# Optimization experiments

Hardware: AMD Instinct MI355X
Metric: run time of the kernel (lower is better)

## Reference

```python
import jax, jax.numpy as jnp
import numpy as np

S, B, E, H, NQ, V, T = 128, 128, 64, 8, 8, 30000, 12
N_RAND_OPS = 30


def _build_random_layer(n_wires, n_ops=N_RAND_OPS, seed=1234):
    # Deterministic stand-in for tq.RandomLayer(n_ops=30): random fixed-angle
    # rotations and CNOTs over the wires.
    rng = np.random.RandomState(seed)
    ops = []
    for _ in range(n_ops):
        kind = rng.randint(4)
        if kind == 3 and n_wires >= 2:
            c = int(rng.randint(n_wires))
            t = int(rng.randint(n_wires - 1))
            if t >= c:
                t += 1
            ops.append(('cnot', c, t, 0.0))
        else:
            g = ('rx', 'ry', 'rz')[kind % 3]
            ops.append((g, int(rng.randint(n_wires)), -1, float(rng.uniform(0.0, 2 * np.pi))))
    return ops

_RAND_OPS = _build_random_layer(H)


def _apply_rot(state, kind, theta, w):
    # state: (N, 2, 2, ..., 2); wire w lives on axis w+1. theta: scalar or (N,).
    th = jnp.asarray(theta, jnp.float32)
    if th.ndim == 1:
        th = th.reshape((-1,) + (1,) * (state.ndim - 2))
    th = th / 2
    a0 = jnp.take(state, 0, axis=w + 1)
    a1 = jnp.take(state, 1, axis=w + 1)
    c, s = jnp.cos(th), jnp.sin(th)
    if kind == 'rx':
        n0, n1 = c * a0 - 1j * s * a1, -1j * s * a0 + c * a1
    elif kind == 'ry':
        n0, n1 = c * a0 - s * a1, s * a0 + c * a1
    else:  # rz
        p = jnp.exp(-1j * th)
        n0, n1 = p * a0, jnp.conj(p) * a1
    return jnp.stack([n0, n1], axis=w + 1)


def _apply_cnot(state, c, t):
    s0 = jnp.take(state, 0, axis=c + 1)
    s1 = jnp.take(state, 1, axis=c + 1)
    t_ax = t + 1 if t < c else t  # target axis after removing control axis
    s1 = jnp.flip(s1, axis=t_ax)
    return jnp.stack([s0, s1], axis=c + 1)


def _measure_z(state):
    probs = jnp.real(state * jnp.conj(state))
    n = state.ndim - 1
    zs = []
    for w in range(n):
        d = jnp.take(probs, 0, axis=w + 1) - jnp.take(probs, 1, axis=w + 1)
        zs.append(d.sum(axis=tuple(range(1, d.ndim))))
    return jnp.stack(zs, axis=1)  # (N, n_wires)


def setup_inputs() -> dict:
    key = jax.random.key(0)
    ks = jax.random.split(key, 10)
    fan_lin = E + H
    return {
        'emb': jax.random.normal(ks[0], (V, E), jnp.float32),
        'Win': jax.random.normal(ks[1], (4, NQ, fan_lin), jnp.float32) / np.sqrt(fan_lin),
        'b_in': jax.random.normal(ks[2], (4, NQ), jnp.float32) * 0.1,
        'phi': jax.random.uniform(ks[3], (4, NQ), jnp.float32, 0.0, 2 * np.pi),
        'Wout': jax.random.normal(ks[4], (4, H, NQ), jnp.float32) / np.sqrt(NQ),
        'b_out': jax.random.normal(ks[5], (4, H), jnp.float32) * 0.1,
        'phiq': jax.random.uniform(ks[6], (H,), jnp.float32, 0.0, 2 * np.pi),
        'Whead': jax.random.normal(ks[7], (T, H), jnp.float32) / np.sqrt(H),
        'b_head': jax.random.normal(ks[8], (T,), jnp.float32) * 0.1,
        'sentence': jax.random.randint(ks[9], (S, B), 0, V, jnp.int64),
    }


def reference(emb, Win, b_in, phi, Wout, b_out, phiq, Whead, b_head, sentence):
    embeds = emb[sentence]  # (S, B, E)
    bsz = sentence.shape[1]
    h0 = jnp.zeros((bsz, H), emb.dtype)
    c0 = jnp.zeros_like(h0)

    def step(carry, x):
        hx, cx = carry
        comb = jnp.concatenate([x, hx], axis=1)  # (B, E+H)
        # QGate closed form: RX(z_i) encode + trainable RX(phi_i) + CNOT chain
        # gives <Z_k> = prod_{j<=k} cos(z_j + phi_j).
        z = jnp.einsum('bf,gqf->bgq', comb, Win) + b_in + phi  # (B,4,NQ)
        q = jnp.cumprod(jnp.cos(z), axis=-1)
        pre = jnp.einsum('bgq,ghq->bgh', q, Wout) + b_out      # (B,4,H)
        f = jax.nn.sigmoid(pre[:, 0])
        i = jax.nn.sigmoid(pre[:, 1])
        g = jnp.tanh(pre[:, 2])
        o = jax.nn.sigmoid(pre[:, 3])
        cx = f * cx + i * g
        hx = o * jnp.tanh(cx)
        return (hx, cx), hx

    _, outs = jax.lax.scan(step, (h0, c0), embeds)  # (S, B, H)
    flat = outs.transpose(1, 0, 2).reshape(-1, H)   # (B*S, H) batch-major (as in source)

    # QFC head: statevector simulation over H wires
    n = H
    N = flat.shape[0]
    state = jnp.zeros((N, 2 ** n), jnp.complex64).at[:, 0].set(1.0)
    state = state.reshape((N,) + (2,) * n)
    for w in range(n):
        state = _apply_rot(state, 'ry', flat[:, w], w)
    for name, a, b, ang in _RAND_OPS:
        if name == 'cnot':
            state = _apply_cnot(state, a, b)
        else:
            state = _apply_rot(state, name, ang, a)
    for w in range(n):
        state = _apply_rot(state, 'rx', phiq[w], w)
    zexp = _measure_z(state)                        # (B*S, H)
    logits = zexp @ Whead.T + b_head
    # faithful to source: view batch-major flat tensor as (seq, batch, T)
    logits = logits.reshape(S, B, T)
    return jax.nn.log_softmax(logits, axis=2)
```

## Files before the change

### kernel.cpp

```cpp
#include <hip/hip_runtime.h>
#include <math.h>
#include <stdint.h>

#define S_    128
#define B_    128
#define E_    64
#define H_    8
#define T_    12
#define FAN_  72
#define NOPS_ 30
#define MAXG_ 30
#define NROWS_ (S_ * B_)

constexpr double CT_PI = 3.14159265358979323846;

constexpr double ct_cos(double x) {
    double t = 1.0, s = 1.0, x2 = x * x;
    for (int k = 1; k <= 20; k++) { t *= -x2 / ((2.0*k - 1.0) * (2.0*k)); s += t; }
    return s;
}
constexpr double ct_sin(double x) {
    double t = x, s = x, x2 = x * x;
    for (int k = 1; k <= 20; k++) { t *= -x2 / ((2.0*k) * (2.0*k + 1.0)); s += t; }
    return s;
}

constexpr void ct_mmul(const double* A, const double* B, double* C) {
    for (int i = 0; i < 2; i++)
        for (int j = 0; j < 2; j++) {
            double rr = 0.0, ii = 0.0;
            for (int k = 0; k < 2; k++) {
                double ar = A[(i*2+k)*2], ai = A[(i*2+k)*2+1];
                double br = B[(k*2+j)*2], bi = B[(k*2+j)*2+1];
                rr += ar*br - ai*bi;
                ii += ar*bi + ai*br;
            }
            C[(i*2+j)*2] = rr; C[(i*2+j)*2+1] = ii;
        }
}

struct CTC {
    int n;
    int type[MAXG_];
    int w1[MAXG_];
    int w2[MAXG_];
    double U[MAXG_][8];
    double initM[8][8];
    double endM[8][8];
};

constexpr CTC build_ct() {
    uint32_t mt[624] = {};
    int idx = 624;
    {
        uint32_t s = 1234u;
        for (int i = 0; i < 624; i++) {
            mt[i] = s;
            s = 1812433253u * (s ^ (s >> 30)) + (uint32_t)i + 1u;
        }
    }
    auto nextf = [&]() -> uint32_t {
        if (idx >= 624) {
            for (int i = 0; i < 624; i++) {
                uint32_t y = (mt[i] & 0x80000000u) | (mt[(i+1)%624] & 0x7fffffffu);
                uint32_t v = mt[(i+397)%624] ^ (y >> 1);
                mt[i] = (y & 1u) ? (v ^ 0x9908b0dfu) : v;
            }
            idx = 0;
        }
        uint32_t y = mt[idx++];
        y ^= y >> 11;
        y ^= (y << 7)  & 0x9d2c5680u;
        y ^= (y << 15) & 0xefc60000u;
        y ^= y >> 18;
        return y;
    };
    auto randint = [&](uint32_t n) -> uint32_t {
        uint32_t rng = n - 1u, mask = rng;
        mask |= mask >> 1; mask |= mask >> 2; mask |= mask >> 4;
        mask |= mask >> 8; mask |= mask >> 16;
        uint32_t v = 0;
        do { v = nextf() & mask; } while (v > rng);
        return v;
    };
    auto uniform2pi = [&]() -> double {
        uint32_t a = nextf() >> 5;
        uint32_t b = nextf() >> 6;
        double d = ((double)a * 67108864.0 + (double)b) / 9007199254740992.0;
        return 2.0 * CT_PI * d;
    };

    int kindA[NOPS_] = {}, aA[NOPS_] = {}, bA[NOPS_] = {};
    double UA[NOPS_][8] = {};
    for (int i = 0; i < NOPS_; i++) {
        uint32_t kind = randint(4);
        if (kind == 3u) {
            int c = (int)randint(8);
            int t = (int)randint(7);
            if (t >= c) t += 1;
            kindA[i] = 1; aA[i] = c; bA[i] = t;
            UA[i][0] = 1.0; UA[i][6] = 1.0;
        } else {
            int g = (int)(kind % 3u);
            int w = (int)randint(8);
            double th = uniform2pi();
            double c = ct_cos(0.5 * th), s = ct_sin(0.5 * th);
            kindA[i] = 0; aA[i] = w; bA[i] = -1;
            if (g == 0)      { UA[i][0]=c;  UA[i][3]=-s; UA[i][5]=-s; UA[i][6]=c; }
            else if (g == 1) { UA[i][0]=c;  UA[i][2]=-s; UA[i][4]= s; UA[i][6]=c; }
            else             { UA[i][0]=c;  UA[i][1]=-s; UA[i][6]= c; UA[i][7]=s; }
        }
    }

    int ikind[MAXG_] = {}, ia[MAXG_] = {}, ib[MAXG_] = {};
    double iU[MAXG_][8] = {};
    int cnt = 0;
    double initM[8][8] = {}, endM[8][8] = {};
    for (int w = 0; w < 8; w++) { initM[w][0] = 1.0; initM[w][6] = 1.0;
                                  endM[w][0]  = 1.0; endM[w][6]  = 1.0; }

    for (int oi = 0; oi < NOPS_; oi++) {
        if (kindA[oi] == 0) {
            int w = aA[oi], k = cnt - 1;
            bool merged = false;
            while (k >= 0) {
                if (ikind[k] == 0) {
                    if (ia[k] == w) {
                        double tmp[8] = {};
                        ct_mmul(UA[oi], iU[k], tmp);
                        for (int j = 0; j < 8; j++) iU[k][j] = tmp[j];
                        merged = true; break;
                    }
                    k--;
                } else {
                    if (w == ia[k] || w == ib[k]) break;
                    k--;
                }
            }
            if (merged) continue;
            if (k < 0) {
                double tmp[8] = {};
                ct_mmul(UA[oi], initM[w], tmp);
                for (int j = 0; j < 8; j++) initM[w][j] = tmp[j];
                continue;
            }
            ikind[cnt] = 0; ia[cnt] = w; ib[cnt] = -1;
            for (int j = 0; j < 8; j++) iU[cnt][j] = UA[oi][j];
            cnt++;
        } else {
            int c = aA[oi], t2 = bA[oi], k = cnt - 1;
            bool cancelled = false;
            while (k >= 0) {
                if (ikind[k] == 0) {
                    int w = ia[k];
                    if (w == c || w == t2) break;
                    k--;
                } else {
                    int c2 = ia[k], tt = ib[k];
                    if (c2 == c && tt == t2) {
                        for (int m = k; m < cnt - 1; m++) {
                            ikind[m] = ikind[m+1]; ia[m] = ia[m+1]; ib[m] = ib[m+1];
                            for (int j = 0; j < 8; j++) iU[m][j] = iU[m+1][j];
                        }
                        cnt--; cancelled = true; break;
                    }
                    if (c2 != t2 && tt != c) k--;
                    else break;
                }
            }
            if (!cancelled) {
                ikind[cnt] = 1; ia[cnt] = c; ib[cnt] = t2;
                for (int j = 0; j < 8; j++) iU[cnt][j] = 0.0;
                iU[cnt][0] = 1.0; iU[cnt][6] = 1.0;
                cnt++;
            }
        }
    }
    bool blocked[8] = {};
    for (int k = cnt - 1; k >= 0; k--) {
        if (ikind[k] == 0) {
            int w = ia[k];
            if (!blocked[w]) {
                double tmp[8] = {};
                ct_mmul(endM[w], iU[k], tmp);
                for (int j = 0; j < 8; j++) endM[w][j] = tmp[j];
                for (int m = k; m < cnt - 1; m++) {
                    ikind[m] = ikind[m+1]; ia[m] = ia[m+1]; ib[m] = ib[m+1];
                    for (int j = 0; j < 8; j++) iU[m][j] = iU[m+1][j];
                }
                cnt--;
            }
        } else {
            blocked[ia[k]] = true; blocked[ib[k]] = true;
        }
    }

    CTC q = {};
    q.n = cnt;
    for (int i = 0; i < cnt; i++) {
        q.type[i] = ikind[i]; q.w1[i] = ia[i]; q.w2[i] = ib[i];
        for (int j = 0; j < 8; j++) q.U[i][j] = iU[i][j];
    }
    for (int w = 0; w < 8; w++)
        for (int j = 0; j < 8; j++) { q.initM[w][j] = initM[w][j]; q.endM[w][j] = endM[w][j]; }
    return q;
}

constexpr CTC CIRC = build_ct();

#define LOG2E_  1.4426950408889634f
#define LOG2E2_ 2.8853900817779268f

__device__ __forceinline__ float fast_sigmoid(float x) {
    return __builtin_amdgcn_rcpf(1.f + __builtin_amdgcn_exp2f(-LOG2E_ * x));
}
__device__ __forceinline__ float fast_tanh(float x) {
    return 1.f - 2.f * __builtin_amdgcn_rcpf(1.f + __builtin_amdgcn_exp2f(LOG2E2_ * x));
}

template<int CTRL>
__device__ __forceinline__ float dppf(float x) {
    union { float f; int i; } u, r;
    u.f = x;
    r.i = __builtin_amdgcn_update_dpp(0, u.i, CTRL, 0xF, 0xF, true);
    return r.f;
}

template<int M>
__device__ __forceinline__ float lane_xor(float x, int lane) {
    if constexpr (M == 1)  return dppf<0xB1>(x);
    else if constexpr (M == 2) return dppf<0x4E>(x);
    else if constexpr (M == 4) {
        float a = dppf<0x104>(x);
        float b = dppf<0x114>(x);
        return (lane & 4) ? b : a;
    }
    else if constexpr (M == 8) return dppf<0x128>(x);
    else return __shfl_xor(x, M, 64);
}

template<int W>
__device__ __forceinline__ float exch(float x, int lane) {
    if constexpr (W == 0) return __shfl_xor(x, 32, 64);
    else if constexpr (W == 1) return __shfl_xor(x, 16, 64);
    else if constexpr (W == 2) return lane_xor<8>(x, lane);
    else if constexpr (W == 3) return lane_xor<4>(x, lane);
    else if constexpr (W == 4) return lane_xor<2>(x, lane);
    else return lane_xor<1>(x, lane);
}

template<int W>
__device__ __forceinline__ int qbit_ct(int lane, int j) {
    if constexpr (W < 6) return (lane >> (5 - W)) & 1;
    else if constexpr (W == 6) return (j >> 1) & 1;
    else return j & 1;
}

__device__ __forceinline__ void pair_rt(float u0, float u1, float u2, float u3,
                                        float u4, float u5, float u6, float u7,
                                        float& a0r, float& a0i, float& a1r, float& a1i) {
    float n0r = u0*a0r - u1*a0i + u2*a1r - u3*a1i;
    float n0i = u0*a0i + u1*a0r + u2*a1i + u3*a1r;
    float n1r = u4*a0r - u5*a0i + u6*a1r - u7*a1i;
    float n1i = u4*a0i + u5*a0r + u6*a1i + u7*a1r;
    a0r = n0r; a0i = n0i; a1r = n1r; a1i = n1i;
}

template<int W>
__device__ __forceinline__ void gate_rt(float u0, float u1, float u2, float u3,
                                        float u4, float u5, float u6, float u7,
                                        int lane, float ar[4], float ai[4]) {
    if constexpr (W < 6) {
        const int b = (lane >> (5 - W)) & 1;
        const float dr  = b ? u6 : u0;
        const float di  = b ? u7 : u1;
        const float onr = b ? u4 : u2;
        const float oni = b ? u5 : u3;
        #pragma unroll
        for (int j = 0; j < 4; j++) {
            float br = exch<W>(ar[j], lane);
            float bi = exch<W>(ai[j], lane);
            float nr = dr * ar[j] - di * ai[j] + onr * br - oni * bi;
            float ni = dr * ai[j] + di * ar[j] + onr * bi + oni * br;
            ar[j] = nr; ai[j] = ni;
        }
    } else if constexpr (W == 6) {
        pair_rt(u0,u1,u2,u3,u4,u5,u6,u7, ar[0], ai[0], ar[2], ai[2]);
        pair_rt(u0,u1,u2,u3,u4,u5,u6,u7, ar[1], ai[1], ar[3], ai[3]);
    } else {
        pair_rt(u0,u1,u2,u3,u4,u5,u6,u7, ar[0], ai[0], ar[1], ai[1]);
        pair_rt(u0,u1,u2,u3,u4,u5,u6,u7, ar[2], ai[2], ar[3], ai[3]);
    }
}

template<int CW, int TW>
__device__ __forceinline__ void cnot_ct(int lane, float ar[4], float ai[4]) {
    if constexpr (TW < 6) {
        #pragma unroll
        for (int j = 0; j < 4; j++) {
            float br = exch<TW>(ar[j], lane);
            float bi = exch<TW>(ai[j], lane);
            int ctrl = qbit_ct<CW>(lane, j);
            ar[j] = ctrl ? br : ar[j];
            ai[j] = ctrl ? bi : ai[j];
        }
    } else if constexpr (TW == 6) {
        int cA = qbit_ct<CW>(lane, 0), cB = qbit_ct<CW>(lane, 1);
        float n0r = cA ? ar[2] : ar[0], n0i = cA ? ai[2] : ai[0];
        float n2r = cA ? ar[0] : ar[2], n2i = cA ? ai[0] : ai[2];
        float n1r = cB ? ar[3] : ar[1], n1i = cB ? ai[3] : ai[1];
        float n3r = cB ? ar[1] : ar[3], n3i = cB ? ai[1] : ai[3];
        ar[0]=n0r; ai[0]=n0i; ar[1]=n1r; ai[1]=n1i;
        ar[2]=n2r; ai[2]=n2i; ar[3]=n3r; ai[3]=n3i;
    } else {
        int cA = qbit_ct<CW>(lane, 0), cB = qbit_ct<CW>(lane, 2);
        float n0r = cA ? ar[1] : ar[0], n0i = cA ? ai[1] : ai[0];
        float n1r = cA ? ar[0] : ar[1], n1i = cA ? ai[0] : ai[1];
        float n2r = cB ? ar[3] : ar[2], n2i = cB ? ai[3] : ai[2];
        float n3r = cB ? ar[2] : ar[3], n3i = cB ? ai[2] : ai[3];
        ar[0]=n0r; ai[0]=n0i; ar[1]=n1r; ai[1]=n1i;
        ar[2]=n2r; ai[2]=n2i; ar[3]=n3r; ai[3]=n3i;
    }
}

template<int I>
__device__ __forceinline__ void gate_op(int lane, float ar[4], float ai[4]) {
    constexpr int w = CIRC.w1[I];
    constexpr float u0 = (float)CIRC.U[I][0], u1 = (float)CIRC.U[I][1];
    constexpr float u2 = (float)CIRC.U[I][2], u3 = (float)CIRC.U[I][3];
    constexpr float u4 = (float)CIRC.U[I][4], u5 = (float)CIRC.U[I][5];
    constexpr float u6 = (float)CIRC.U[I][6], u7 = (float)CIRC.U[I][7];
    gate_rt<w>(u0,u1,u2,u3,u4,u5,u6,u7, lane, ar, ai);
}

template<int I>
__device__ __forceinline__ void run_ops(int lane, float ar[4], float ai[4]) {
    if constexpr (I < CIRC.n) {
        if constexpr (CIRC.type[I] == 0) gate_op<I>(lane, ar, ai);
        else cnot_ct<CIRC.w1[I], CIRC.w2[I]>(lane, ar, ai);
        run_ops<I + 1>(lane, ar, ai);
    }
}

struct V2 { float r0, i0, r1, i1; };
template<int W>
__device__ __forceinline__ V2 init_wire(float th) {
    constexpr float m0 = (float)CIRC.initM[W][0], m1 = (float)CIRC.initM[W][1];
    constexpr float m2 = (float)CIRC.initM[W][2], m3 = (float)CIRC.initM[W][3];
    constexpr float m4 = (float)CIRC.initM[W][4], m5 = (float)CIRC.initM[W][5];
    constexpr float m6 = (float)CIRC.initM[W][6], m7 = (float)CIRC.initM[W][7];
    float c = __cosf(th), s = __sinf(th);
    V2 v;
    v.r0 = m0*c + m2*s; v.i0 = m1*c + m3*s;
    v.r1 = m4*c + m6*s; v.i1 = m5*c + m7*s;
    return v;
}

template<int W>
__device__ __forceinline__ void final_wire(float c, float s, int lane,
                                           float ar[4], float ai[4]) {
    constexpr float E0 = (float)CIRC.endM[W][0], E1 = (float)CIRC.endM[W][1];
    constexpr float E2 = (float)CIRC.endM[W][2], E3 = (float)CIRC.endM[W][3];
    constexpr float E4 = (float)CIRC.endM[W][4], E5 = (float)CIRC.endM[W][5];
    constexpr float E6 = (float)CIRC.endM[W][6], E7 = (float)CIRC.endM[W][7];
    float F0 =  c*E0 + s*E5;
    float F1 =  c*E1 - s*E4;
    float F2 =  c*E2 + s*E7;
    float F3 =  c*E3 - s*E6;
    float F4 =  s*E1 + c*E4;
    float F5 = -s*E0 + c*E5;
    float F6 =  s*E3 + c*E6;
    float F7 = -s*E2 + c*E7;
    gate_rt<W>(F0,F1,F2,F3,F4,F5,F6,F7, lane, ar, ai);
}

__device__ __forceinline__ void bcast8(float v, int lane, float h[8]) {
    float p  = lane_xor<1>(v, lane);
    float a0 = (lane & 1) ? p : v;
    float a1 = (lane & 1) ? v : p;
    float q0 = lane_xor<2>(a0, lane);
    float q1 = lane_xor<2>(a1, lane);
    float b0 = (lane & 2) ? q0 : a0;
    float b1 = (lane & 2) ? q1 : a1;
    float b2 = (lane & 2) ? a0 : q0;
    float b3 = (lane & 2) ? a1 : q1;
    float r0 = lane_xor<4>(b0, lane);
    float r1 = lane_xor<4>(b1, lane);
    float r2 = lane_xor<4>(b2, lane);
    float r3 = lane_xor<4>(b3, lane);
    h[0] = (lane & 4) ? r0 : b0;  h[1] = (lane & 4) ? r1 : b1;
    h[2] = (lane & 4) ? r2 : b2;  h[3] = (lane & 4) ? r3 : b3;
    h[4] = (lane & 4) ? b0 : r0;  h[5] = (lane & 4) ? b1 : r1;
    h[6] = (lane & 4) ? b2 : r2;  h[7] = (lane & 4) ? b3 : r3;
}

__device__ __forceinline__ void bcast8_s2(float v, int lane, float h[8]) {
    float p  = lane_xor<2>(v, lane);
    float a0 = (lane & 2) ? p : v;
    float a1 = (lane & 2) ? v : p;
    float q0 = lane_xor<4>(a0, lane);
    float q1 = lane_xor<4>(a1, lane);
    float b0 = (lane & 4) ? q0 : a0;
    float b1 = (lane & 4) ? q1 : a1;
    float b2 = (lane & 4) ? a0 : q0;
    float b3 = (lane & 4) ? a1 : q1;
    float r0 = lane_xor<8>(b0, lane);
    float r1 = lane_xor<8>(b1, lane);
    float r2 = lane_xor<8>(b2, lane);
    float r3 = lane_xor<8>(b3, lane);
    h[0] = (lane & 8) ? r0 : b0;  h[1] = (lane & 8) ? r1 : b1;
    h[2] = (lane & 8) ? r2 : b2;  h[3] = (lane & 8) ? r3 : b3;
    h[4] = (lane & 8) ? b0 : r0;  h[5] = (lane & 8) ? b1 : r1;
    h[6] = (lane & 8) ? b2 : r2;  h[7] = (lane & 8) ? b3 : r3;
}

__device__ __forceinline__ void qfc_row(const float th[8],
    float cq[8], float sq[8], int lane,
    const float* __restrict__ Whead, const float* __restrict__ b_head,
    float* __restrict__ outrow)
{
    float ar[4], ai[4];
    {
        V2 v0 = init_wire<0>(th[0]);
        V2 v1 = init_wire<1>(th[1]);
        V2 v2 = init_wire<2>(th[2]);
        V2 v3 = init_wire<3>(th[3]);
        V2 v4 = init_wire<4>(th[4]);
        V2 v5 = init_wire<5>(th[5]);
        V2 v6 = init_wire<6>(th[6]);
        V2 v7 = init_wire<7>(th[7]);
        float Pr = 1.f, Pi = 0.f;
        {
            int bit = (lane >> 5) & 1;
            float er = bit ? v0.r1 : v0.r0, ei = bit ? v0.i1 : v0.i0;
            float nr = Pr*er - Pi*ei, ni = Pr*ei + Pi*er; Pr = nr; Pi = ni;
        }
        {
            int bit = (lane >> 4) & 1;
            float er = bit ? v1.r1 : v1.r0, ei = bit ? v1.i1 : v1.i0;
            float nr = Pr*er - Pi*ei, ni = Pr*ei + Pi*er; Pr = nr; Pi = ni;
        }
        {
            int bit = (lane >> 3) & 1;
            float er = bit ? v2.r1 : v2.r0, ei = bit ? v2.i1 : v2.i0;
            float nr = Pr*er - Pi*ei, ni = Pr*ei + Pi*er; Pr = nr; Pi = ni;
        }
        {
            int bit = (lane >> 2) & 1;
            float er = bit ? v3.r1 : v3.r0, ei = bit ? v3.i1 : v3.i0;
            float nr = Pr*er - Pi*ei, ni = Pr*ei + Pi*er; Pr = nr; Pi = ni;
        }
        {
            int bit = (lane >> 1) & 1;
            float er = bit ? v4.r1 : v4.r0, ei = bit ? v4.i1 : v4.i0;
            float nr = Pr*er - Pi*ei, ni = Pr*ei + Pi*er; Pr = nr; Pi = ni;
        }
        {
            int bit = lane & 1;
            float er = bit ? v5.r1 : v5.r0, ei = bit ? v5.i1 : v5.i0;
            float nr = Pr*er - Pi*ei, ni = Pr*ei + Pi*er; Pr = nr; Pi = ni;
        }
        float t0r = Pr*v6.r0 - Pi*v6.i0, t0i = Pr*v6.i0 + Pi*v6.r0;
        float t1r = Pr*v6.r1 - Pi*v6.i1, t1i = Pr*v6.i1 + Pi*v6.r1;
        ar[0] = t0r*v7.r0 - t0i*v7.i0;  ai[0] = t0r*v7.i0 + t0i*v7.r0;
        ar[1] = t0r*v7.r1 - t0i*v7.i1;  ai[1] = t0r*v7.i1 + t0i*v7.r1;
        ar[2] = t1r*v7.r0 - t1i*v7.i0;  ai[2] = t1r*v7.i0 + t1i*v7.r0;
        ar[3] = t1r*v7.r1 - t1i*v7.i1;  ai[3] = t1r*v7.i1 + t1i*v7.r1;
    }

    run_ops<0>(lane, ar, ai);

    final_wire<0>(cq[0], sq[0], lane, ar, ai);
    final_wire<1>(cq[1], sq[1], lane, ar, ai);
    final_wire<2>(cq[2], sq[2], lane, ar, ai);
    final_wire<3>(cq[3], sq[3], lane, ar, ai);
    final_wire<4>(cq[4], sq[4], lane, ar, ai);
    final_wire<5>(cq[5], sq[5], lane, ar, ai);
    final_wire<6>(cq[6], sq[6], lane, ar, ai);
    final_wire<7>(cq[7], sq[7], lane, ar, ai);

    float p0 = ar[0]*ar[0] + ai[0]*ai[0];
    float p1 = ar[1]*ar[1] + ai[1]*ai[1];
    float p2 = ar[2]*ar[2] + ai[2]*ai[2];
    float p3 = ar[3]*ar[3] + ai[3]*ai[3];
    float pt = p0 + p1 + p2 + p3;
    float a6 = p0 + p1 - p2 - p3;
    float a7 = p0 - p1 + p2 - p3;
    {
        float tv;
        tv = lane_xor<1>(pt, lane);  pt = (lane & 1)  ? (tv - pt) : (tv + pt);
        tv = lane_xor<2>(pt, lane);  pt = (lane & 2)  ? (tv - pt) : (tv + pt);
        tv = lane_xor<4>(pt, lane);  pt = (lane & 4)  ? (tv - pt) : (tv + pt);
        tv = lane_xor<8>(pt, lane);  pt = (lane & 8)  ? (tv - pt) : (tv + pt);
        tv = lane_xor<16>(pt, lane); pt = (lane & 16) ? (tv - pt) : (tv + pt);
        tv = lane_xor<32>(pt, lane); pt = (lane & 32) ? (tv - pt) : (tv + pt);
        a6 += lane_xor<1>(a6, lane);  a6 += lane_xor<2>(a6, lane);
        a6 += lane_xor<4>(a6, lane);  a6 += lane_xor<8>(a6, lane);
        a6 += lane_xor<16>(a6, lane); a6 += lane_xor<32>(a6, lane);
        a7 += lane_xor<1>(a7, lane);  a7 += lane_xor<2>(a7, lane);
        a7 += lane_xor<4>(a7, lane);  a7 += lane_xor<8>(a7, lane);
        a7 += lane_xor<16>(a7, lane); a7 += lane_xor<32>(a7, lane);
    }
    float zl[8];
    zl[0] = __shfl(pt, 32, 64);
    zl[1] = __shfl(pt, 16, 64);
    zl[2] = __shfl(pt, 8, 64);
    zl[3] = __shfl(pt, 4, 64);
    zl[4] = __shfl(pt, 2, 64);
    zl[5] = __shfl(pt, 1, 64);
    zl[6] = a6;
    zl[7] = a7;

    float logit = -1e30f;
    if (lane < T_) {
        logit = b_head[lane];
        #pragma unroll
        for (int w = 0; w < 8; w++)
            logit = fmaf(zl[w], Whead[lane * 8 + w], logit);
    }
    float mx = logit;
    mx = fmaxf(mx, lane_xor<1>(mx, lane));
    mx = fmaxf(mx, lane_xor<2>(mx, lane));
    mx = fmaxf(mx, lane_xor<4>(mx, lane));
    mx = fmaxf(mx, lane_xor<8>(mx, lane));
    float e = (lane < T_) ? __expf(logit - mx) : 0.f;
    float se = e;
    se += lane_xor<1>(se, lane);
    se += lane_xor<2>(se, lane);
    se += lane_xor<4>(se, lane);
    se += lane_xor<8>(se, lane);
    if (lane < T_)
        outrow[lane] = logit - mx - __logf(se);
}

__global__ __launch_bounds__(256) void k_lstm(
    const float* __restrict__ emb,
    const int* __restrict__ sentence,
    const float* __restrict__ Win,
    const float* __restrict__ b_in,
    const float* __restrict__ phi,
    const float* __restrict__ Wout,
    const float* __restrict__ b_out,
    float* __restrict__ angles)
{
    __shared__ float zxs[S_][32];

    const int t  = threadIdx.x;
    const int hw = t >> 5;
    const int l  = t & 31;
    const int b  = blockIdx.x;

    {
        const float4* w4 = (const float4*)(Win + l * FAN_);
        const float cb = b_in[l] + phi[l];

        #pragma unroll
        for (int kk = 0; kk < 4; kk++) {
            const int sb = hw * 16 + kk * 4;
            const float4* e4_0 = (const float4*)(emb + sentence[(sb + 0) * B_ + b] * E_);
            const float4* e4_1 = (const float4*)(emb + sentence[(sb + 1) * B_ + b] * E_);
            const float4* e4_2 = (const float4*)(emb + sentence[(sb + 2) * B_ + b] * E_);
            const float4* e4_3 = (const float4*)(emb + sentence[(sb + 3) * B_ + b] * E_);
            float a0 = cb, a1 = cb, a2 = cb, a3 = cb;
            #pragma unroll
            for (int f = 0; f < 16; f++) {
                float4 wv = w4[f];
                float4 x0 = e4_0[f];
                float4 x1 = e4_1[f];
                float4 x2 = e4_2[f];
                float4 x3 = e4_3[f];
                a0 = fmaf(x0.x, wv.x, a0); a0 = fmaf(x0.y, wv.y, a0);
                a0 = fmaf(x0.z, wv.z, a0); a0 = fmaf(x0.w, wv.w, a0);
                a1 = fmaf(x1.x, wv.x, a1); a1 = fmaf(x1.y, wv.y, a1);
                a1 = fmaf(x1.z, wv.z, a1); a1 = fmaf(x1.w, wv.w, a1);
                a2 = fmaf(x2.x, wv.x, a2); a2 = fmaf(x2.y, wv.y, a2);
                a2 = fmaf(x2.z, wv.z, a2); a2 = fmaf(x2.w, wv.w, a2);
                a3 = fmaf(x3.x, wv.x, a3); a3 = fmaf(x3.y, wv.y, a3);
                a3 = fmaf(x3.z, wv.z, a3); a3 = fmaf(x3.w, wv.w, a3);
            }
            zxs[sb + 0][l] = a0;
            zxs[sb + 1][l] = a1;
            zxs[sb + 2][l] = a2;
            zxs[sb + 3][l] = a3;
        }
    }
    __syncthreads();

    if (t < 16) {
        const int j = t & 1;
        const int q = t >> 1;
        const int rowA = j * 8 + q;
        const int rowB = (j + 2) * 8 + q;

        float whA[8], whB[8], woA[8], woB[8];
        #pragma unroll
        for (int k = 0; k < 8; k++) {
            whA[k] = Win[rowA * FAN_ + 64 + k];
            whB[k] = Win[rowB * FAN_ + 64 + k];
            woA[k] = Wout[rowA * 8 + k];
            woB[k] = Wout[rowB * 8 + k];
        }
        const float boA = b_out[rowA];
        const float boB = b_out[rowB];

        float hxv[8];
        #pragma unroll
        for (int k = 0; k < 8; k++) hxv[k] = 0.f;
        float cx = 0.f;

        float zAn = zxs[0][rowA];
        float zBn = zxs[0][rowB];

        for (int s = 0; s < S_; s++) {
            float zA = zAn, zB = zBn;
            const int sn = (s + 1) & (S_ - 1);
            zAn = zxs[sn][rowA];
            zBn = zxs[sn][rowB];

            float za0 = zA, za1 = 0.f, zb0 = zB, zb1 = 0.f;
            #pragma unroll
            for (int k = 0; k < 4; k++) {
                za0 = fmaf(whA[k], hxv[k], za0);
                za1 = fmaf(whA[k + 4], hxv[k + 4], za1);
                zb0 = fmaf(whB[k], hxv[k], zb0);
                zb1 = fmaf(whB[k + 4], hxv[k + 4], zb1);
            }
            float qcA = __cosf(za0 + za1);
            float qcB = __cosf(zb0 + zb1);

            {
                float uA = dppf<0x112>(qcA), uB = dppf<0x112>(qcB);
                if (q >= 1) { qcA *= uA; qcB *= uB; }
                uA = dppf<0x114>(qcA); uB = dppf<0x114>(qcB);
                if (q >= 2) { qcA *= uA; qcB *= uB; }
                uA = dppf<0x118>(qcA); uB = dppf<0x118>(qcB);
                if (q >= 4) { qcA *= uA; qcB *= uB; }
            }

            float cA[8], cB[8];
            bcast8_s2(qcA, t, cA);
            bcast8_s2(qcB, t, cB);

            float pa0 = boA, pa1 = 0.f, pb0 = boB, pb1 = 0.f;
            #pragma unroll
            for (int k = 0; k < 4; k++) {
                pa0 = fmaf(woA[k], cA[k], pa0);
                pa1 = fmaf(woA[k + 4], cA[k + 4], pa1);
                pb0 = fmaf(woB[k], cB[k], pb0);
                pb1 = fmaf(woB[k + 4], cB[k + 4], pb1);
            }
            float preA = pa0 + pa1;
            float preB = pb0 + pb1;

            float prA = dppf<0xB1>(preA);
            float prB = dppf<0xB1>(preB);
            float p0 = j ? prA  : preA;
            float p1 = j ? preA : prA;
            float p2 = j ? prB  : preB;
            float p3 = j ? preB : prB;

            float f_ = fast_sigmoid(p0);
            float i_ = fast_sigmoid(p1);
            float g_ = fast_tanh(p2);
            float o_ = fast_sigmoid(p3);
            cx = fmaf(f_, cx, i_ * g_);
            float hnew = o_ * fast_tanh(cx);

            if (j == 0) angles[(b * S_ + s) * 8 + q] = hnew;
            bcast8_s2(hnew, t, hxv);
        }
    }
}

__global__ __launch_bounds__(256) void k_qfc(
    const float* __restrict__ angles,
    const float* __restrict__ phiq,
    const float* __restrict__ Whead,
    const float* __restrict__ b_head,
    float* __restrict__ out)
{
    const int t      = threadIdx.x;
    const int lane   = t & 63;
    const int waveId = blockIdx.x * 4 + (t >> 6);

    float cq[8], sq[8];
    #pragma unroll
    for (int w = 0; w < 8; w++) {
        float ph = phiq[w] * 0.5f;
        cq[w] = __cosf(ph); sq[w] = __sinf(ph);
    }

    #pragma unroll
    for (int rr = 0; rr < 2; rr++) {
        const int row = waveId * 2 + rr;
        float th[8];
        #pragma unroll
        for (int w = 0; w < 8; w++) th[w] = angles[row * 8 + w] * 0.5f;
        qfc_row(th, cq, sq, lane, Whead, b_head, out + row * T_);
    }
}

__global__ __launch_bounds__(1024) void k_fused(
    const float* __restrict__ emb,
    const int* __restrict__ sentence,
    const float* __restrict__ Win,
    const float* __restrict__ b_in,
    const float* __restrict__ phi,
    const float* __restrict__ Wout,
    const float* __restrict__ b_out,
    const float* __restrict__ phiq,
    const float* __restrict__ Whead,
    const float* __restrict__ b_head,
    float* __restrict__ out)
{
    __shared__ float zxs[S_][32];
    __shared__ float sang[S_][8];

    const int t     = threadIdx.x;
    const int wave  = t >> 6;
    const int lane  = t & 63;
    const int half  = lane >> 5;
    const int l     = lane & 31;
    const int b     = blockIdx.x >> 1;
    const int half3 = blockIdx.x & 1;

    {
        const float4* w4 = (const float4*)(Win + l * FAN_);
        const float cb = b_in[l] + phi[l];
        const int s0 = wave * 8 + 0 + half;
        const int s1 = wave * 8 + 2 + half;
        const int s2 = wave * 8 + 4 + half;
        const int s3 = wave * 8 + 6 + half;
        const float4* e4_0 = (const float4*)(emb + sentence[s0 * B_ + b] * E_);
        const float4* e4_1 = (const float4*)(emb + sentence[s1 * B_ + b] * E_);
        const float4* e4_2 = (const float4*)(emb + sentence[s2 * B_ + b] * E_);
        const float4* e4_3 = (const float4*)(emb + sentence[s3 * B_ + b] * E_);
        float a0 = cb, a1 = cb, a2 = cb, a3 = cb;
        #pragma unroll
        for (int f = 0; f < 16; f++) {
            float4 wv = w4[f];
            float4 x0 = e4_0[f];
            float4 x1 = e4_1[f];
            float4 x2 = e4_2[f];
            float4 x3 = e4_3[f];
            a0 = fmaf(x0.x, wv.x, a0); a0 = fmaf(x0.y, wv.y, a0);
            a0 = fmaf(x0.z, wv.z, a0); a0 = fmaf(x0.w, wv.w, a0);
            a1 = fmaf(x1.x, wv.x, a1); a1 = fmaf(x1.y, wv.y, a1);
            a1 = fmaf(x1.z, wv.z, a1); a1 = fmaf(x1.w, wv.w, a1);
            a2 = fmaf(x2.x, wv.x, a2); a2 = fmaf(x2.y, wv.y, a2);
            a2 = fmaf(x2.z, wv.z, a2); a2 = fmaf(x2.w, wv.w, a2);
            a3 = fmaf(x3.x, wv.x, a3); a3 = fmaf(x3.y, wv.y, a3);
            a3 = fmaf(x3.z, wv.z, a3); a3 = fmaf(x3.w, wv.w, a3);
        }
        zxs[s0][l] = a0;
        zxs[s1][l] = a1;
        zxs[s2][l] = a2;
        zxs[s3][l] = a3;
    }
    __syncthreads();

    if (t < 32) {
        const int g = t >> 3;
        const int h = t & 7;
        const int q = t & 7;
        float wh[8], wo[8];
        #pragma unroll
        for (int k = 0; k < 8; k++) wh[k] = Win[t * FAN_ + 64 + k];
        #pragma unroll
        for (int k = 0; k < 8; k++) wo[k] = Wout[(g * 8 + h) * 8 + k];
        const float bo = b_out[g * 8 + h];

        float hxv[8];
        #pragma unroll
        for (int k = 0; k < 8; k++) hxv[k] = 0.f;
        float cx = 0.f;

        for (int s = 0; s < S_; s++) {
            float z = zxs[s][t];
            #pragma unroll
            for (int k = 0; k < 8; k++) z = fmaf(wh[k], hxv[k], z);

            float qc = __cosf(z);
            float u1 = dppf<0x111>(qc); qc = (q >= 1) ? qc * u1 : qc;
            float u2 = dppf<0x112>(qc); qc = (q >= 2) ? qc * u2 : qc;
            float u4 = dppf<0x114>(qc); qc = (q >= 4) ? qc * u4 : qc;

            float qch[8];
            bcast8(qc, t, qch);
            float pre = bo;
            #pragma unroll
            for (int qq = 0; qq < 8; qq++) pre = fmaf(wo[qq], qch[qq], pre);

            float e1 = lane_xor<8>(pre, t);
            float e2 = __shfl_xor(pre, 16, 64);
            float e3 = __shfl_xor(e1, 16, 64);
            float p0 = (g==0)?pre:(g==1)?e1:(g==2)?e2:e3;
            float p1 = (g==1)?pre:(g==0)?e1:(g==3)?e2:e3;
            float p2 = (g==2)?pre:(g==3)?e1:(g==0)?e2:e3;
            float p3 = (g==3)?pre:(g==2)?e1:(g==1)?e2:e3;

            float f_ = fast_sigmoid(p0);
            float i_ = fast_sigmoid(p1);
            float g_ = fast_tanh(p2);
            float o_ = fast_sigmoid(p3);
            cx = fmaf(f_, cx, i_ * g_);
            float hnew = o_ * fast_tanh(cx);

            if (t < 8) sang[s][t] = hnew;
            bcast8(hnew, t, hxv);
        }
    }
    __syncthreads();

    float cq[8], sq[8];
    #pragma unroll
    for (int w = 0; w < 8; w++) {
        float ph = phiq[w] * 0.5f;
        cq[w] = __cosf(ph); sq[w] = __sinf(ph);
    }

    for (int r = 0; r < 4; r++) {
        const int s = half3 * 64 + wave * 4 + r;
        float th[8];
        #pragma unroll
        for (int w = 0; w < 8; w++) th[w] = sang[s][w] * 0.5f;
        qfc_row(th, cq, sq, lane, Whead, b_head, out + (b * S_ + s) * T_);
    }
}

extern "C" void kernel_launch(void* const* d_in, const int* in_sizes, int n_in,
                              void* d_out, int out_size, void* d_ws, size_t ws_size,
                              hipStream_t stream)
{
    (void)in_sizes; (void)n_in; (void)out_size;
    const float* emb    = (const float*)d_in[0];
    const float* Win    = (const float*)d_in[1];
    const float* b_in   = (const float*)d_in[2];
    const float* phi    = (const float*)d_in[3];
    const float* Wout   = (const float*)d_in[4];
    const float* b_out  = (const float*)d_in[5];
    const float* phiq   = (const float*)d_in[6];
    const float* Whead  = (const float*)d_in[7];
    const float* b_head = (const float*)d_in[8];
    const int* sentence = (const int*)d_in[9];
    float* out          = (float*)d_out;

    const size_t need = (size_t)NROWS_ * 8 * sizeof(float);
    if (ws_size >= need) {
        float* angles = (float*)d_ws;
        hipLaunchKernelGGL(k_lstm, dim3(B_), dim3(256), 0, stream,
                           emb, sentence, Win, b_in, phi, Wout, b_out, angles);
        hipLaunchKernelGGL(k_qfc, dim3(NROWS_ / 8), dim3(256), 0, stream,
                           angles, phiq, Whead, b_head, out);
    } else {
        hipLaunchKernelGGL(k_fused, dim3(2 * B_), dim3(1024), 0, stream,
                           emb, sentence, Win, b_in, phi, Wout, b_out,
                           phiq, Whead, b_head, out);
    }
}
```

Measured before the change: 181.0 us.

## Fuse LSTM and QFC into one kernel with intra-block producer-consumer overlap

Replaces the two-kernel path (LSTM writing angles to workspace, then a separate QFC kernel) with a single 1024-thread block per batch element. Wave 0 runs the sequential LSTM recurrence and publishes progress through a shared-memory counter every four steps. The other 15 waves spin on that counter and run the quantum-circuit head for finished timesteps while the recurrence continues. This removes the second launch and the global round trip and hides QFC work behind the serial LSTM chain, at the cost of only 128 blocks and spin-waiting waves. The DPP helper now passes the source value as the old operand instead of zero.

```diff
diff --git a/kernel.cpp b/kernel.cpp
--- a/kernel.cpp
+++ b/kernel.cpp
@@ -222,7 +222,7 @@
 __device__ __forceinline__ float dppf(float x) {
     union { float f; int i; } u, r;
     u.f = x;
-    r.i = __builtin_amdgcn_update_dpp(0, u.i, CTRL, 0xF, 0xF, true);
+    r.i = __builtin_amdgcn_update_dpp(u.i, u.i, CTRL, 0xF, 0xF, true);
     return r.f;
 }
 
@@ -372,26 +372,6 @@
     float F6 =  s*E3 + c*E6;
     float F7 = -s*E2 + c*E7;
     gate_rt<W>(F0,F1,F2,F3,F4,F5,F6,F7, lane, ar, ai);
-}
-
-__device__ __forceinline__ void bcast8(float v, int lane, float h[8]) {
-    float p  = lane_xor<1>(v, lane);
-    float a0 = (lane & 1) ? p : v;
-    float a1 = (lane & 1) ? v : p;
-    float q0 = lane_xor<2>(a0, lane);
-    float q1 = lane_xor<2>(a1, lane);
-    float b0 = (lane & 2) ? q0 : a0;
-    float b1 = (lane & 2) ? q1 : a1;
-    float b2 = (lane & 2) ? a0 : q0;
-    float b3 = (lane & 2) ? a1 : q1;
-    float r0 = lane_xor<4>(b0, lane);
-    float r1 = lane_xor<4>(b1, lane);
-    float r2 = lane_xor<4>(b2, lane);
-    float r3 = lane_xor<4>(b3, lane);
-    h[0] = (lane & 4) ? r0 : b0;  h[1] = (lane & 4) ? r1 : b1;
-    h[2] = (lane & 4) ? r2 : b2;  h[3] = (lane & 4) ? r3 : b3;
-    h[4] = (lane & 4) ? b0 : r0;  h[5] = (lane & 4) ? b1 : r1;
-    h[6] = (lane & 4) ? b2 : r2;  h[7] = (lane & 4) ? b3 : r3;
 }
 
 __device__ __forceinline__ void bcast8_s2(float v, int lane, float h[8]) {
@@ -533,174 +513,7 @@
         outrow[lane] = logit - mx - __logf(se);
 }
 
-__global__ __launch_bounds__(256) void k_lstm(
-    const float* __restrict__ emb,
-    const int* __restrict__ sentence,
-    const float* __restrict__ Win,
-    const float* __restrict__ b_in,
-    const float* __restrict__ phi,
-    const float* __restrict__ Wout,
-    const float* __restrict__ b_out,
-    float* __restrict__ angles)
-{
-    __shared__ float zxs[S_][32];
-
-    const int t  = threadIdx.x;
-    const int hw = t >> 5;
-    const int l  = t & 31;
-    const int b  = blockIdx.x;
-
-    {
-        const float4* w4 = (const float4*)(Win + l * FAN_);
-        const float cb = b_in[l] + phi[l];
-
-        #pragma unroll
-        for (int kk = 0; kk < 4; kk++) {
-            const int sb = hw * 16 + kk * 4;
-            const float4* e4_0 = (const float4*)(emb + sentence[(sb + 0) * B_ + b] * E_);
-            const float4* e4_1 = (const float4*)(emb + sentence[(sb + 1) * B_ + b] * E_);
-            const float4* e4_2 = (const float4*)(emb + sentence[(sb + 2) * B_ + b] * E_);
-            const float4* e4_3 = (const float4*)(emb + sentence[(sb + 3) * B_ + b] * E_);
-            float a0 = cb, a1 = cb, a2 = cb, a3 = cb;
-            #pragma unroll
-            for (int f = 0; f < 16; f++) {
-                float4 wv = w4[f];
-                float4 x0 = e4_0[f];
-                float4 x1 = e4_1[f];
-                float4 x2 = e4_2[f];
-                float4 x3 = e4_3[f];
-                a0 = fmaf(x0.x, wv.x, a0); a0 = fmaf(x0.y, wv.y, a0);
-                a0 = fmaf(x0.z, wv.z, a0); a0 = fmaf(x0.w, wv.w, a0);
-                a1 = fmaf(x1.x, wv.x, a1); a1 = fmaf(x1.y, wv.y, a1);
-                a1 = fmaf(x1.z, wv.z, a1); a1 = fmaf(x1.w, wv.w, a1);
-                a2 = fmaf(x2.x, wv.x, a2); a2 = fmaf(x2.y, wv.y, a2);
-                a2 = fmaf(x2.z, wv.z, a2); a2 = fmaf(x2.w, wv.w, a2);
-                a3 = fmaf(x3.x, wv.x, a3); a3 = fmaf(x3.y, wv.y, a3);
-                a3 = fmaf(x3.z, wv.z, a3); a3 = fmaf(x3.w, wv.w, a3);
-            }
-            zxs[sb + 0][l] = a0;
-            zxs[sb + 1][l] = a1;
-            zxs[sb + 2][l] = a2;
-            zxs[sb + 3][l] = a3;
-        }
-    }
-    __syncthreads();
-
-    if (t < 16) {
-        const int j = t & 1;
-        const int q = t >> 1;
-        const int rowA = j * 8 + q;
-        const int rowB = (j + 2) * 8 + q;
-
-        float whA[8], whB[8], woA[8], woB[8];
-        #pragma unroll
-        for (int k = 0; k < 8; k++) {
-            whA[k] = Win[rowA * FAN_ + 64 + k];
-            whB[k] = Win[rowB * FAN_ + 64 + k];
-            woA[k] = Wout[rowA * 8 + k];
-            woB[k] = Wout[rowB * 8 + k];
-        }
-        const float boA = b_out[rowA];
-        const float boB = b_out[rowB];
-
-        float hxv[8];
-        #pragma unroll
-        for (int k = 0; k < 8; k++) hxv[k] = 0.f;
-        float cx = 0.f;
-
-        float zAn = zxs[0][rowA];
-        float zBn = zxs[0][rowB];
-
-        for (int s = 0; s < S_; s++) {
-            float zA = zAn, zB = zBn;
-            const int sn = (s + 1) & (S_ - 1);
-            zAn = zxs[sn][rowA];
-            zBn = zxs[sn][rowB];
-
-            float za0 = zA, za1 = 0.f, zb0 = zB, zb1 = 0.f;
-            #pragma unroll
-            for (int k = 0; k < 4; k++) {
-                za0 = fmaf(whA[k], hxv[k], za0);
-                za1 = fmaf(whA[k + 4], hxv[k + 4], za1);
-                zb0 = fmaf(whB[k], hxv[k], zb0);
-                zb1 = fmaf(whB[k + 4], hxv[k + 4], zb1);
-            }
-            float qcA = __cosf(za0 + za1);
-            float qcB = __cosf(zb0 + zb1);
-
-            {
-                float uA = dppf<0x112>(qcA), uB = dppf<0x112>(qcB);
-                if (q >= 1) { qcA *= uA; qcB *= uB; }
-                uA = dppf<0x114>(qcA); uB = dppf<0x114>(qcB);
-                if (q >= 2) { qcA *= uA; qcB *= uB; }
-                uA = dppf<0x118>(qcA); uB = dppf<0x118>(qcB);
-                if (q >= 4) { qcA *= uA; qcB *= uB; }
-            }
-
-            float cA[8], cB[8];
-            bcast8_s2(qcA, t, cA);
-            bcast8_s2(qcB, t, cB);
-
-            float pa0 = boA, pa1 = 0.f, pb0 = boB, pb1 = 0.f;
-            #pragma unroll
-            for (int k = 0; k < 4; k++) {
-                pa0 = fmaf(woA[k], cA[k], pa0);
-                pa1 = fmaf(woA[k + 4], cA[k + 4], pa1);
-                pb0 = fmaf(woB[k], cB[k], pb0);
-                pb1 = fmaf(woB[k + 4], cB[k + 4], pb1);
-            }
-            float preA = pa0 + pa1;
-            float preB = pb0 + pb1;
-
-            float prA = dppf<0xB1>(preA);
-            float prB = dppf<0xB1>(preB);
-            float p0 = j ? prA  : preA;
-            float p1 = j ? preA : prA;
-            float p2 = j ? prB  : preB;
-            float p3 = j ? preB : prB;
-
-            float f_ = fast_sigmoid(p0);
-            float i_ = fast_sigmoid(p1);
-            float g_ = fast_tanh(p2);
-            float o_ = fast_sigmoid(p3);
-            cx = fmaf(f_, cx, i_ * g_);
-            float hnew = o_ * fast_tanh(cx);
-
-            if (j == 0) angles[(b * S_ + s) * 8 + q] = hnew;
-            bcast8_s2(hnew, t, hxv);
-        }
-    }
-}
-
-__global__ __launch_bounds__(256) void k_qfc(
-    const float* __restrict__ angles,
-    const float* __restrict__ phiq,
-    const float* __restrict__ Whead,
-    const float* __restrict__ b_head,
-    float* __restrict__ out)
-{
-    const int t      = threadIdx.x;
-    const int lane   = t & 63;
-    const int waveId = blockIdx.x * 4 + (t >> 6);
-
-    float cq[8], sq[8];
-    #pragma unroll
-    for (int w = 0; w < 8; w++) {
-        float ph = phiq[w] * 0.5f;
-        cq[w] = __cosf(ph); sq[w] = __sinf(ph);
-    }
-
-    #pragma unroll
-    for (int rr = 0; rr < 2; rr++) {
-        const int row = waveId * 2 + rr;
-        float th[8];
-        #pragma unroll
-        for (int w = 0; w < 8; w++) th[w] = angles[row * 8 + w] * 0.5f;
-        qfc_row(th, cq, sq, lane, Whead, b_head, out + row * T_);
-    }
-}
-
-__global__ __launch_bounds__(1024) void k_fused(
+__global__ __launch_bounds__(1024) void k_all(
     const float* __restrict__ emb,
     const int* __restrict__ sentence,
     const float* __restrict__ Win,
@@ -715,26 +528,25 @@
 {
     __shared__ float zxs[S_][32];
     __shared__ float sang[S_][8];
-
-    const int t     = threadIdx.x;
-    const int wave  = t >> 6;
-    const int lane  = t & 63;
-    const int half  = lane >> 5;
-    const int l     = lane & 31;
-    const int b     = blockIdx.x >> 1;
-    const int half3 = blockIdx.x & 1;
+    __shared__ int   sprog;
+
+    const int t    = threadIdx.x;
+    const int wave = t >> 6;
+    const int lane = t & 63;
+    const int b    = blockIdx.x;
+
+    if (t == 0) sprog = 0;
 
     {
+        const int hw = t >> 5;
+        const int l  = t & 31;
         const float4* w4 = (const float4*)(Win + l * FAN_);
         const float cb = b_in[l] + phi[l];
-        const int s0 = wave * 8 + 0 + half;
-        const int s1 = wave * 8 + 2 + half;
-        const int s2 = wave * 8 + 4 + half;
-        const int s3 = wave * 8 + 6 + half;
-        const float4* e4_0 = (const float4*)(emb + sentence[s0 * B_ + b] * E_);
-        const float4* e4_1 = (const float4*)(emb + sentence[s1 * B_ + b] * E_);
-        const float4* e4_2 = (const float4*)(emb + sentence[s2 * B_ + b] * E_);
-        const float4* e4_3 = (const float4*)(emb + sentence[s3 * B_ + b] * E_);
+        const int sb = hw * 4;
+        const float4* e4_0 = (const float4*)(emb + sentence[(sb + 0) * B_ + b] * E_);
+        const float4* e4_1 = (const float4*)(emb + sentence[(sb + 1) * B_ + b] * E_);
+        const float4* e4_2 = (const float4*)(emb + sentence[(sb + 2) * B_ + b] * E_);
+        const float4* e4_3 = (const float4*)(emb + sentence[(sb + 3) * B_ + b] * E_);
         float a0 = cb, a1 = cb, a2 = cb, a3 = cb;
         #pragma unroll
         for (int f = 0; f < 16; f++) {
@@ -752,79 +564,118 @@
             a3 = fmaf(x3.x, wv.x, a3); a3 = fmaf(x3.y, wv.y, a3);
             a3 = fmaf(x3.z, wv.z, a3); a3 = fmaf(x3.w, wv.w, a3);
         }
-        zxs[s0][l] = a0;
-        zxs[s1][l] = a1;
-        zxs[s2][l] = a2;
-        zxs[s3][l] = a3;
+        zxs[sb + 0][l] = a0;
+        zxs[sb + 1][l] = a1;
+        zxs[sb + 2][l] = a2;
+        zxs[sb + 3][l] = a3;
     }
     __syncthreads();
 
-    if (t < 32) {
-        const int g = t >> 3;
-        const int h = t & 7;
-        const int q = t & 7;
-        float wh[8], wo[8];
+    if (wave == 0) {
+        if (lane < 16) {
+            const int j = t & 1;
+            const int q = t >> 1;
+            const int rowA = j * 8 + q;
+            const int rowB = (j + 2) * 8 + q;
+
+            float whA[8], whB[8], woA[8], woB[8];
+            #pragma unroll
+            for (int k = 0; k < 8; k++) {
+                whA[k] = Win[rowA * FAN_ + 64 + k];
+                whB[k] = Win[rowB * FAN_ + 64 + k];
+                woA[k] = Wout[rowA * 8 + k];
+                woB[k] = Wout[rowB * 8 + k];
+            }
+            const float boA = b_out[rowA];
+            const float boB = b_out[rowB];
+
+            float hxv[8];
+            #pragma unroll
+            for (int k = 0; k < 8; k++) hxv[k] = 0.f;
+            float cx = 0.f;
+
+            float zAn = zxs[0][rowA];
+            float zBn = zxs[0][rowB];
+
+            for (int s = 0; s < S_; s++) {
+                float zA = zAn, zB = zBn;
+                const int sn = (s + 1) & (S_ - 1);
+                zAn = zxs[sn][rowA];
+                zBn = zxs[sn][rowB];
+
+                float za0 = zA, za1 = 0.f, zb0 = zB, zb1 = 0.f;
+                #pragma unroll
+                for (int k = 0; k < 4; k++) {
+                    za0 = fmaf(whA[k], hxv[k], za0);
+                    za1 = fmaf(whA[k + 4], hxv[k + 4], za1);
+                    zb0 = fmaf(whB[k], hxv[k], zb0);
+                    zb1 = fmaf(whB[k + 4], hxv[k + 4], zb1);
+                }
+                float qcA = __cosf(za0 + za1);
+                float qcB = __cosf(zb0 + zb1);
+
+                {
+                    float uA = dppf<0x112>(qcA), uB = dppf<0x112>(qcB);
+                    if (q >= 1) { qcA *= uA; qcB *= uB; }
+                    uA = dppf<0x114>(qcA); uB = dppf<0x114>(qcB);
+                    if (q >= 2) { qcA *= uA; qcB *= uB; }
+                    uA = dppf<0x118>(qcA); uB = dppf<0x118>(qcB);
+                    if (q >= 4) { qcA *= uA; qcB *= uB; }
+                }
+
+                float cA[8], cB[8];
+                bcast8_s2(qcA, t, cA);
+                bcast8_s2(qcB, t, cB);
+
+                float pa0 = boA, pa1 = 0.f, pb0 = boB, pb1 = 0.f;
+                #pragma unroll
+                for (int k = 0; k < 4; k++) {
+                    pa0 = fmaf(woA[k], cA[k], pa0);
+                    pa1 = fmaf(woA[k + 4], cA[k + 4], pa1);
+                    pb0 = fmaf(woB[k], cB[k], pb0);
+                    pb1 = fmaf(woB[k + 4], cB[k + 4], pb1);
+                }
+                float preA = pa0 + pa1;
+                float preB = pb0 + pb1;
+
+                float prA = dppf<0xB1>(preA);
+                float prB = dppf<0xB1>(preB);
+                float p0 = j ? prA  : preA;
+                float p1 = j ? preA : prA;
+                float p2 = j ? prB  : preB;
+                float p3 = j ? preB : prB;
+
+                float f_ = fast_sigmoid(p0);
+                float i_ = fast_sigmoid(p1);
+                float g_ = fast_tanh(p2);
+                float o_ = fast_sigmoid(p3);
+                cx = fmaf(f_, cx, i_ * g_);
+                float hnew = o_ * fast_tanh(cx);
+
+                if (j == 0) sang[s][q] = hnew;
+                if ((s & 3) == 3) {
+                    __threadfence_block();
+                    if (t == 0) *(volatile int*)&sprog = s + 1;
+                }
+                bcast8_s2(hnew, t, hxv);
+            }
+        }
+    } else {
+        float cq[8], sq[8];
         #pragma unroll
-        for (int k = 0; k < 8; k++) wh[k] = Win[t * FAN_ + 64 + k];
-        #pragma unroll
-        for (int k = 0; k < 8; k++) wo[k] = Wout[(g * 8 + h) * 8 + k];
-        const float bo = b_out[g * 8 + h];
-
-        float hxv[8];
-        #pragma unroll
-        for (int k = 0; k < 8; k++) hxv[k] = 0.f;
-        float cx = 0.f;
-
-        for (int s = 0; s < S_; s++) {
-            float z = zxs[s][t];
+        for (int w = 0; w < 8; w++) {
+            float ph = phiq[w] * 0.5f;
+            cq[w] = __cosf(ph); sq[w] = __sinf(ph);
+        }
+
+        for (int s = wave - 1; s < S_; s += 15) {
+            while (*(volatile int*)&sprog <= s)
+                __builtin_amdgcn_s_sleep(2);
+            float th[8];
             #pragma unroll
-            for (int k = 0; k < 8; k++) z = fmaf(wh[k], hxv[k], z);
-
-            float qc = __cosf(z);
-            float u1 = dppf<0x111>(qc); qc = (q >= 1) ? qc * u1 : qc;
-            float u2 = dppf<0x112>(qc); qc = (q >= 2) ? qc * u2 : qc;
-            float u4 = dppf<0x114>(qc); qc = (q >= 4) ? qc * u4 : qc;
-
-            float qch[8];
-            bcast8(qc, t, qch);
-            float pre = bo;
-            #pragma unroll
-            for (int qq = 0; qq < 8; qq++) pre = fmaf(wo[qq], qch[qq], pre);
-
-            float e1 = lane_xor<8>(pre, t);
-            float e2 = __shfl_xor(pre, 16, 64);
-            float e3 = __shfl_xor(e1, 16, 64);
-            float p0 = (g==0)?pre:(g==1)?e1:(g==2)?e2:e3;
-            float p1 = (g==1)?pre:(g==0)?e1:(g==3)?e2:e3;
-            float p2 = (g==2)?pre:(g==3)?e1:(g==0)?e2:e3;
-            float p3 = (g==3)?pre:(g==2)?e1:(g==1)?e2:e3;
-
-            float f_ = fast_sigmoid(p0);
-            float i_ = fast_sigmoid(p1);
-            float g_ = fast_tanh(p2);
-            float o_ = fast_sigmoid(p3);
-            cx = fmaf(f_, cx, i_ * g_);
-            float hnew = o_ * fast_tanh(cx);
-
-            if (t < 8) sang[s][t] = hnew;
-            bcast8(hnew, t, hxv);
-        }
-    }
-    __syncthreads();
-
-    float cq[8], sq[8];
-    #pragma unroll
-    for (int w = 0; w < 8; w++) {
-        float ph = phiq[w] * 0.5f;
-        cq[w] = __cosf(ph); sq[w] = __sinf(ph);
-    }
-
-    for (int r = 0; r < 4; r++) {
-        const int s = half3 * 64 + wave * 4 + r;
-        float th[8];
-        #pragma unroll
-        for (int w = 0; w < 8; w++) th[w] = sang[s][w] * 0.5f;
-        qfc_row(th, cq, sq, lane, Whead, b_head, out + (b * S_ + s) * T_);
+            for (int w = 0; w < 8; w++) th[w] = sang[s][w] * 0.5f;
+            qfc_row(th, cq, sq, lane, Whead, b_head, out + (b * S_ + s) * T_);
+        }
     }
 }
 
@@ -832,7 +683,7 @@
                               void* d_out, int out_size, void* d_ws, size_t ws_size,
                               hipStream_t stream)
 {
-    (void)in_sizes; (void)n_in; (void)out_size;
+    (void)in_sizes; (void)n_in; (void)out_size; (void)d_ws; (void)ws_size;
     const float* emb    = (const float*)d_in[0];
     const float* Win    = (const float*)d_in[1];
     const float* b_in   = (const float*)d_in[2];
@@ -845,16 +696,7 @@
     const int* sentence = (const int*)d_in[9];
     float* out          = (float*)d_out;
 
-    const size_t need = (size_t)NROWS_ * 8 * sizeof(float);
-    if (ws_size >= need) {
-        float* angles = (float*)d_ws;
-        hipLaunchKernelGGL(k_lstm, dim3(B_), dim3(256), 0, stream,
-                           emb, sentence, Win, b_in, phi, Wout, b_out, angles);
-        hipLaunchKernelGGL(k_qfc, dim3(NROWS_ / 8), dim3(256), 0, stream,
-                           angles, phiq, Whead, b_head, out);
-    } else {
-        hipLaunchKernelGGL(k_fused, dim3(2 * B_), dim3(1024), 0, stream,
-                           emb, sentence, Win, b_in, phi, Wout, b_out,
-                           phiq, Whead, b_head, out);
-    }
-}
+    hipLaunchKernelGGL(k_all, dim3(B_), dim3(1024), 0, stream,
+                       emb, sentence, Win, b_in, phi, Wout, b_out,
+                       phiq, Whead, b_head, out);
+}
```

Result: faster. 155.7 us (median of 2 runs) (-14.0%).
